# Performance work log

Hardware: AMD Instinct MI355X
Metric: run time of the kernel (lower is better)

## Reference

```python
import jax, jax.numpy as jnp
import numpy as np
from jax import lax

D_MODEL = 1024
D_STATE = 16
D_CONV = 4
EXPAND = 2
D_INNER = EXPAND * D_MODEL           # 2048 (mamba inner)
DT_RANK = (D_MODEL + 15) // 16       # 64
D_FF = 4 * D_MODEL                   # 4096 (SwiGLU hidden)
EPS = 1e-5
B, L = 2, 2048


def setup_inputs() -> dict:
    key = jax.random.key(0)
    ks = jax.random.split(key, 16)
    s = 0.02
    inp = {
        'x': jax.random.normal(ks[0], (B, L, D_MODEL), jnp.float32),
        'norm1_w': jnp.ones((D_MODEL,), jnp.float32),
        'norm2_w': jnp.ones((D_MODEL,), jnp.float32),
        # Mamba params (torch Linear convention: y = x @ W.T)
        'in_proj_w': s * jax.random.normal(ks[1], (2 * D_INNER, D_MODEL), jnp.float32),
        'conv_w': s * jax.random.normal(ks[2], (D_INNER, 1, D_CONV), jnp.float32),
        'conv_b': jnp.zeros((D_INNER,), jnp.float32),
        'x_proj_w': s * jax.random.normal(ks[3], (DT_RANK + 2 * D_STATE, D_INNER), jnp.float32),
        'dt_proj_w': s * jax.random.normal(ks[4], (D_INNER, DT_RANK), jnp.float32),
        'dt_proj_b': jax.random.uniform(ks[5], (D_INNER,), jnp.float32, -4.0, -2.0),
        'A_log': jnp.log(jnp.broadcast_to(jnp.arange(1, D_STATE + 1, dtype=jnp.float32), (D_INNER, D_STATE))),
        'D': jnp.ones((D_INNER,), jnp.float32),
        'out_proj_w': s * jax.random.normal(ks[6], (D_MODEL, D_INNER), jnp.float32),
        # SwiGLU MLP
        'w1': s * jax.random.normal(ks[7], (D_FF, D_MODEL), jnp.float32),
        'w2': s * jax.random.normal(ks[8], (D_FF, D_MODEL), jnp.float32),
        'w3': s * jax.random.normal(ks[9], (D_MODEL, D_FF), jnp.float32),
    }
    return inp


def _rmsnorm(x, w, eps=EPS):
    return x * lax.rsqrt(jnp.mean(x * x, axis=-1, keepdims=True) + eps) * w


def _mamba(x, in_proj_w, conv_w, conv_b, x_proj_w, dt_proj_w, dt_proj_b, A_log, Dp, out_proj_w):
    # x: (B, L, d_model)
    xz = x @ in_proj_w.T                       # (B, L, 2*d_inner)
    u, z = jnp.split(xz, 2, axis=-1)           # each (B, L, d_inner)
    # causal depthwise conv1d over time
    u_nch = u.transpose(0, 2, 1)               # (B, d_inner, L)
    u_conv = lax.conv_general_dilated(
        u_nch, conv_w, window_strides=(1,), padding=[(D_CONV - 1, 0)],
        dimension_numbers=('NCH', 'OIH', 'NCH'), feature_group_count=D_INNER)
    u_conv = u_conv + conv_b[None, :, None]
    u_act = jax.nn.silu(u_conv.transpose(0, 2, 1))   # (B, L, d_inner)
    # input-dependent dt, B, C
    proj = u_act @ x_proj_w.T                  # (B, L, dt_rank + 2*d_state)
    dt_r, Bm, Cm = jnp.split(proj, [DT_RANK, DT_RANK + D_STATE], axis=-1)
    dt = jax.nn.softplus(dt_r @ dt_proj_w.T + dt_proj_b)   # (B, L, d_inner)
    A = -jnp.exp(A_log)                        # (d_inner, d_state)
    dA = jnp.exp(jnp.einsum('bld,dn->bldn', dt, A))
    dBu = jnp.einsum('bld,bln,bld->bldn', dt, Bm, u_act)
    def step(h, inputs):
        dA_t, dBu_t = inputs                   # (B, d_inner, d_state)
        h = dA_t * h + dBu_t
        return h, h
    h0 = jnp.zeros((x.shape[0], D_INNER, D_STATE), x.dtype)
    _, hs = lax.scan(step, h0, (dA.transpose(1, 0, 2, 3), dBu.transpose(1, 0, 2, 3)))
    y = jnp.einsum('lbdn,bln->bld', hs, Cm) + u_act * Dp   # (B, L, d_inner)
    y = y * jax.nn.silu(z)
    return y @ out_proj_w.T                    # (B, L, d_model)


def reference(x, norm1_w, norm2_w, in_proj_w, conv_w, conv_b, x_proj_w,
              dt_proj_w, dt_proj_b, A_log, D, out_proj_w, w1, w2, w3):
    # residual + RMSNorm + Mamba (dropout = eval-mode identity)
    h = x + _mamba(_rmsnorm(x, norm1_w), in_proj_w, conv_w, conv_b,
                   x_proj_w, dt_proj_w, dt_proj_b, A_log, D, out_proj_w)
    # residual + RMSNorm + SwiGLU MLP
    xn = _rmsnorm(h, norm2_w)
    mlp = (jax.nn.silu(xn @ w1.T) * (xn @ w2.T)) @ w3.T
    return h + mlp
```

## Files before the change

### kernel.cpp

```cpp
#include <hip/hip_runtime.h>
#include <hip/hip_bf16.h>

#define TOKS 4096
#define DM   1024
#define DI   2048
#define DST  16
#define DTR  64
#define DFF  4096
#define PROJ_LD 128

#define NC    32
#define CHUNK 64

typedef __bf16 bf16x8 __attribute__((ext_vector_type(8)));
typedef float  f32x4  __attribute__((ext_vector_type(4)));

__device__ __forceinline__ __bf16 f2bf(float f) {
  union { float f; unsigned u; } v; v.f = f;
  unsigned r = v.u + 0x7fffu + ((v.u >> 16) & 1u);
  union { unsigned short s; __bf16 b; } o; o.s = (unsigned short)(r >> 16);
  return o.b;
}
__device__ __forceinline__ float siluf(float x) { return x / (1.f + __expf(-x)); }
__device__ __forceinline__ float softplusf(float x) { return x > 20.f ? x : log1pf(__expf(x)); }

__device__ __forceinline__ void gl2lds16(const void* g, void* l) {
  __builtin_amdgcn_global_load_lds((const __attribute__((address_space(1))) void*)g,
                                   (__attribute__((address_space(3))) void*)l, 16, 0, 0);
}

struct CvtArgs {
  const float* src[5];
  __bf16*      dst[5];
  int nblk[6];
};

__global__ __launch_bounds__(256) void cvt_bf16_kernel(CvtArgs a) {
  int blk = blockIdx.x;
  int seg = 0;
#pragma unroll
  for (int s = 1; s < 5; s++) if (blk >= a.nblk[s]) seg = s;
  size_t base = (size_t)(blk - a.nblk[seg]) * 2048 + threadIdx.x * 8;
  const float* src = a.src[seg] + base;
  __bf16*      dst = a.dst[seg] + base;
  float4 v0 = *(const float4*)src;
  float4 v1 = *(const float4*)(src + 4);
  union { __bf16 b[8]; uint4 u; } t;
  t.b[0]=f2bf(v0.x); t.b[1]=f2bf(v0.y); t.b[2]=f2bf(v0.z); t.b[3]=f2bf(v0.w);
  t.b[4]=f2bf(v1.x); t.b[5]=f2bf(v1.y); t.b[6]=f2bf(v1.z); t.b[7]=f2bf(v1.w);
  *(uint4*)dst = t.u;
}

__global__ __launch_bounds__(256) void cvt_w12_kernel(const float* __restrict__ w1,
                                                      const float* __restrict__ w2,
                                                      __bf16* __restrict__ dst) {
  int blk = blockIdx.x;
  int isw2 = blk >> 11;
  int b = blk & 2047;
  int r = b * 2 + (threadIdx.x >> 7);
  int col = (threadIdx.x & 127) * 8;
  const float* src = (isw2 ? w2 : w1) + (size_t)r * DM + col;
  int dr = (r >> 4) * 32 + (r & 15) + isw2 * 16;
  float4 v0 = *(const float4*)src;
  float4 v1 = *(const float4*)(src + 4);
  union { __bf16 b[8]; uint4 u; } t;
  t.b[0]=f2bf(v0.x); t.b[1]=f2bf(v0.y); t.b[2]=f2bf(v0.z); t.b[3]=f2bf(v0.w);
  t.b[4]=f2bf(v1.x); t.b[5]=f2bf(v1.y); t.b[6]=f2bf(v1.z); t.b[7]=f2bf(v1.w);
  *(uint4*)&dst[(size_t)dr * DM + col] = t.u;
}

__global__ __launch_bounds__(256) void rmsnorm_kernel(const float* __restrict__ x,
                                                      const float* __restrict__ w,
                                                      __bf16* __restrict__ out) {
  int row = blockIdx.x;
  const float* xr = x + (size_t)row * DM;
  float4 v = ((const float4*)xr)[threadIdx.x];
  float ss = v.x*v.x + v.y*v.y + v.z*v.z + v.w*v.w;
#pragma unroll
  for (int o = 32; o > 0; o >>= 1) ss += __shfl_xor(ss, o);
  __shared__ float sred[4];
  if ((threadIdx.x & 63) == 0) sred[threadIdx.x >> 6] = ss;
  __syncthreads();
  float tot = sred[0] + sred[1] + sred[2] + sred[3];
  float scale = rsqrtf(tot * (1.f / DM) + 1e-5f);
  float4 wv = ((const float4*)w)[threadIdx.x];
  union { __bf16 b[4]; ushort4 u; } o;
  o.b[0] = f2bf(v.x * scale * wv.x);
  o.b[1] = f2bf(v.y * scale * wv.y);
  o.b[2] = f2bf(v.z * scale * wv.z);
  o.b[3] = f2bf(v.w * scale * wv.w);
  *(ushort4*)&out[(size_t)row * DM + threadIdx.x * 4] = o.u;
}

template<int BM, int EPI, int SWAP, int KK, int Z, int LDA, int LDB, int LDC>
__global__ __launch_bounds__(256, BM == 256 ? 2 : 1) void gemm2(
    const void* __restrict__ Ap, const __bf16* __restrict__ Bp,
    void* __restrict__ Cp, const void* __restrict__ auxp)
{
  constexpr int FM = BM / 32;
  constexpr int AI = BM / 64;
  constexpr int kPer = KK / Z;
  __shared__ __bf16 sA[BM * 32];
  __shared__ __bf16 sB[128 * 32];
  const int tid  = threadIdx.x;
  const int wave = tid >> 6, lane = tid & 63;
  const int bm = SWAP ? blockIdx.x : blockIdx.y;
  const int bn = SWAP ? blockIdx.y : blockIdx.x;
  const int m0 = bm * BM, n0 = bn * 128;
  const int wr = wave >> 1, wc = wave & 1;
  const int frow = lane & 15, fq = lane >> 4;

  f32x4 acc[FM][4] = {};

  const int kBeg = (Z > 1) ? blockIdx.z * kPer : 0;
  const int kEnd = kBeg + kPer;

  const int lrow = lane >> 2;
  const int lcol = (lane & 3) * 8;

  for (int kt = kBeg; kt < kEnd; kt += 32) {
#pragma unroll
    for (int q = 0; q < AI; q++) {
      int idx = wave * AI + q;
      gl2lds16((const __bf16*)Ap + (size_t)(m0 + idx * 16 + lrow) * LDA + kt + lcol,
               &sA[idx * 512]);
    }
#pragma unroll
    for (int q = 0; q < 2; q++) {
      int idx = wave * 2 + q;
      gl2lds16(Bp + (size_t)(n0 + idx * 16 + lrow) * LDB + kt + lcol, &sB[idx * 512]);
    }
    __syncthreads();

    bf16x8 afr[FM], bfr[4];
#pragma unroll
    for (int i = 0; i < FM; i++)
      afr[i] = *(const bf16x8*)&sA[(wr * (BM/2) + i * 16 + frow) * 32 + fq * 8];
#pragma unroll
    for (int j = 0; j < 4; j++)
      bfr[j] = *(const bf16x8*)&sB[(wc * 64 + j * 16 + frow) * 32 + fq * 8];
#pragma unroll
    for (int i = 0; i < FM; i++)
#pragma unroll
      for (int j = 0; j < 4; j++)
        acc[i][j] = __builtin_amdgcn_mfma_f32_16x16x32_bf16(afr[i], bfr[j], acc[i][j], 0, 0, 0);
    __syncthreads();
  }

  const float* auxf = (const float*)auxp;
#pragma unroll
  for (int i = 0; i < FM; i++) {
    int gr = m0 + wr * (BM/2) + i * 16 + fq * 4;
#pragma unroll
    for (int j = 0; j < 4; j++) {
      int gc = n0 + wc * 64 + j * 16 + frow;
#pragma unroll
      for (int r = 0; r < 4; r++) {
        float v = acc[i][j][r];
        if (EPI == 6) {
          if (j & 1) {
            int col = (n0 >> 1) + 32 * wc + 16 * (j >> 1) + frow;
            size_t off = (size_t)(gr + r) * LDC + col;
            float g = acc[i][j-1][r];
            ((__bf16*)Cp)[off] = f2bf(siluf(g) * v);
          }
        } else {
          size_t off = (size_t)(gr + r) * LDC + gc;
          if (EPI == 1) ((__bf16*)Cp)[off] = f2bf(v);
          else if (EPI == 2) ((__bf16*)Cp)[off] = f2bf(softplusf(v + auxf[gc]));
          else if (EPI == 3) ((float*)Cp)[off] = v + auxf[off];
          else if (EPI == 7)
            ((float*)Cp)[(size_t)blockIdx.z * (TOKS * PROJ_LD) + off] = v;
        }
      }
    }
  }
}

__global__ __launch_bounds__(256) void xp_reduce_kernel(const float* __restrict__ part,
                                                        float* __restrict__ proj,
                                                        __bf16* __restrict__ projb) {
  int i = blockIdx.x * 256 + threadIdx.x;
  float4 s = ((const float4*)part)[i];
#pragma unroll
  for (int z = 1; z < 8; z++) {
    float4 v = ((const float4*)(part + (size_t)z * TOKS * PROJ_LD))[i];
    s.x += v.x; s.y += v.y; s.z += v.z; s.w += v.w;
  }
  ((float4*)proj)[i] = s;
  int c4 = i & 31;
  if (c4 < 16) {
    int tok = i >> 5;
    union { __bf16 b[4]; ushort4 u; } t;
    t.b[0]=f2bf(s.x); t.b[1]=f2bf(s.y); t.b[2]=f2bf(s.z); t.b[3]=f2bf(s.w);
    *(ushort4*)&projb[(size_t)tok * 64 + c4 * 4] = t.u;
  }
}

__global__ __launch_bounds__(256) void conv_silu_kernel(const __bf16* __restrict__ xz,
                                                        const float* __restrict__ cw,
                                                        const float* __restrict__ cb,
                                                        __bf16* __restrict__ uact) {
  int idx = blockIdx.x * 256 + threadIdx.x;
  int d   = idx & (DI - 1);
  int tok = idx >> 11;
  int l   = tok & 2047;
  float4 wv = *(const float4*)(cw + d * 4);
  const __bf16* up = xz + (size_t)tok * (2 * DI) + d;
  float acc = cb[d];
  if (l >= 3) acc += wv.x * (float)up[-3 * (2 * DI)];
  if (l >= 2) acc += wv.y * (float)up[-2 * (2 * DI)];
  if (l >= 1) acc += wv.z * (float)up[-1 * (2 * DI)];
  acc += wv.w * (float)up[0];
  uact[idx] = f2bf(siluf(acc));
}

__global__ __launch_bounds__(64) void scan_pass1(const __bf16* __restrict__ dt,
                                                 const __bf16* __restrict__ uact,
                                                 const float* __restrict__ proj,
                                                 const float* __restrict__ A_log,
                                                 float* __restrict__ aprod,
                                                 float* __restrict__ hend) {
  int lane = threadIdx.x;
  int d = blockIdx.x * 64 + lane;
  int c = blockIdx.y, b = blockIdx.z;
  float An[16], h[16], ap[16];
  {
    const float4* a4 = (const float4*)(A_log + (size_t)d * 16);
#pragma unroll
    for (int q = 0; q < 4; q++) {
      float4 v = a4[q];
      An[q*4+0] = -__expf(v.x); An[q*4+1] = -__expf(v.y);
      An[q*4+2] = -__expf(v.z); An[q*4+3] = -__expf(v.w);
    }
  }
#pragma unroll
  for (int n = 0; n < 16; n++) { h[n] = 0.f; ap[n] = 1.f; }

  size_t tok = (size_t)b * 2048 + (size_t)c * CHUNK;
  const __bf16* dtp = dt   + tok * DI + d;
  const __bf16* up  = uact + tok * DI + d;
  const float*  pp  = proj + tok * PROJ_LD;

  for (int t = 0; t < CHUNK; t++) {
    float dtv = (float)*dtp;
    float uv  = (float)*up;
    const float4* b4 = (const float4*)(pp + 64);
    float Bv[16];
#pragma unroll
    for (int q = 0; q < 4; q++) {
      float4 v = b4[q];
      Bv[q*4+0]=v.x; Bv[q*4+1]=v.y; Bv[q*4+2]=v.z; Bv[q*4+3]=v.w;
    }
    float du = dtv * uv;
#pragma unroll
    for (int n = 0; n < 16; n++) {
      float dA = __expf(dtv * An[n]);
      ap[n] *= dA;
      h[n] = fmaf(dA, h[n], du * Bv[n]);
    }
    dtp += DI; up += DI; pp += PROJ_LD;
  }

  size_t off = ((size_t)(b * NC + c) * DI + d) * 16;
#pragma unroll
  for (int q = 0; q < 4; q++) {
    *(float4*)(hend  + off + q*4) = make_float4(h[q*4+0],  h[q*4+1],  h[q*4+2],  h[q*4+3]);
    *(float4*)(aprod + off + q*4) = make_float4(ap[q*4+0], ap[q*4+1], ap[q*4+2], ap[q*4+3]);
  }
}

__global__ __launch_bounds__(256) void scan_pass2(const float* __restrict__ aprod,
                                                  const float* __restrict__ hend,
                                                  float* __restrict__ hstart) {
  int idx = blockIdx.x * 256 + threadIdx.x;
  int b  = idx >> 13;
  int r4 = idx & 8191;
  float4 H = make_float4(0.f, 0.f, 0.f, 0.f);
  for (int c = 0; c < NC; c++) {
    size_t off = (size_t)(b * NC + c) * (DI * 16 / 4) + r4;
    ((float4*)hstart)[off] = H;
    float4 a = ((const float4*)aprod)[off];
    float4 e = ((const float4*)hend)[off];
    H.x = fmaf(a.x, H.x, e.x);
    H.y = fmaf(a.y, H.y, e.y);
    H.z = fmaf(a.z, H.z, e.z);
    H.w = fmaf(a.w, H.w, e.w);
  }
}

__global__ __launch_bounds__(64) void scan_pass3(const __bf16* __restrict__ dt,
                                                 const __bf16* __restrict__ uact,
                                                 const float* __restrict__ proj,
                                                 const __bf16* __restrict__ xz,
                                                 const float* __restrict__ A_log,
                                                 const float* __restrict__ Dp,
                                                 const float* __restrict__ hstart,
                                                 __bf16* __restrict__ y) {
  int lane = threadIdx.x;
  int d = blockIdx.x * 64 + lane;
  int c = blockIdx.y, b = blockIdx.z;
  float An[16], h[16];
  {
    const float4* a4 = (const float4*)(A_log + (size_t)d * 16);
#pragma unroll
    for (int q = 0; q < 4; q++) {
      float4 v = a4[q];
      An[q*4+0] = -__expf(v.x); An[q*4+1] = -__expf(v.y);
      An[q*4+2] = -__expf(v.z); An[q*4+3] = -__expf(v.w);
    }
  }
  {
    size_t off = ((size_t)(b * NC + c) * DI + d) * 16;
#pragma unroll
    for (int q = 0; q < 4; q++) {
      float4 v = *(const float4*)(hstart + off + q*4);
      h[q*4+0]=v.x; h[q*4+1]=v.y; h[q*4+2]=v.z; h[q*4+3]=v.w;
    }
  }
  float Dd = Dp[d];

  size_t tok = (size_t)b * 2048 + (size_t)c * CHUNK;
  const __bf16* dtp = dt   + tok * DI + d;
  const __bf16* up  = uact + tok * DI + d;
  const float*  pp  = proj + tok * PROJ_LD;
  const __bf16* zp  = xz   + tok * (2 * DI) + DI + d;
  __bf16*       yp  = y    + tok * DI + d;

  for (int t = 0; t < CHUNK; t++) {
    float dtv = (float)*dtp;
    float uv  = (float)*up;
    float zv  = (float)*zp;
    const float4* b4 = (const float4*)(pp + 64);
    float Bv[16], Cv[16];
#pragma unroll
    for (int q = 0; q < 4; q++) {
      float4 v = b4[q];
      Bv[q*4+0]=v.x; Bv[q*4+1]=v.y; Bv[q*4+2]=v.z; Bv[q*4+3]=v.w;
      float4 w = b4[q + 4];
      Cv[q*4+0]=w.x; Cv[q*4+1]=w.y; Cv[q*4+2]=w.z; Cv[q*4+3]=w.w;
    }
    float du = dtv * uv;
    float p = 0.f;
#pragma unroll
    for (int n = 0; n < 16; n++) {
      float dA = __expf(dtv * An[n]);
      h[n] = fmaf(dA, h[n], du * Bv[n]);
      p = fmaf(h[n], Cv[n], p);
    }
    *yp = f2bf((p + Dd * uv) * siluf(zv));
    dtp += DI; up += DI; pp += PROJ_LD; zp += 2 * DI; yp += DI;
  }
}

extern "C" void kernel_launch(void* const* d_in, const int* in_sizes, int n_in,
                              void* d_out, int out_size, void* d_ws, size_t ws_size,
                              hipStream_t stream) {
  const float* x        = (const float*)d_in[0];
  const float* n1w      = (const float*)d_in[1];
  const float* n2w      = (const float*)d_in[2];
  const float* in_projw = (const float*)d_in[3];
  const float* conv_w   = (const float*)d_in[4];
  const float* conv_b   = (const float*)d_in[5];
  const float* x_projw  = (const float*)d_in[6];
  const float* dt_projw = (const float*)d_in[7];
  const float* dt_projb = (const float*)d_in[8];
  const float* A_log    = (const float*)d_in[9];
  const float* Dp       = (const float*)d_in[10];
  const float* out_projw= (const float*)d_in[11];
  const float* w1       = (const float*)d_in[12];
  const float* w2       = (const float*)d_in[13];
  const float* w3       = (const float*)d_in[14];
  float* out = (float*)d_out;

  char* ws = (char*)d_ws;
  __bf16* xz   = (__bf16*)(ws + 0);
  __bf16* uact = (__bf16*)(ws + 33554432);
  float*  proj = (float*) (ws + 50331648);
  __bf16* dt   = (__bf16*)(ws + 52428800);
  __bf16* yb   = (__bf16*)(ws + 85983232);
  float*  xpp  = (float*) (ws + 85983232);
  float*  h    = (float*) (ws + 102760448);
  __bf16* xn   = (__bf16*)(ws + 119537664);
  __bf16* hid  = xz;
  __bf16* projb = (__bf16*)(ws + 102760448);
  float* aprod  = (float*)(ws + 102760448);
  float* hend   = (float*)(ws + 111149056);
  float* hstart = (float*)(ws + 119537664);
  char* wb = ws + 127926272;
  __bf16* b_in  = (__bf16*)(wb);
  __bf16* b_xp  = (__bf16*)(wb + 8388608);
  __bf16* b_dtp = (__bf16*)(wb + 8912896);
  __bf16* b_out = (__bf16*)(wb + 9175040);
  __bf16* b_w12 = (__bf16*)(wb + 13369344);
  __bf16* b_w3  = (__bf16*)(wb + 30146560);

  hipMemsetAsync(b_xp, 0, 128 * 2048 * sizeof(__bf16), stream);

  CvtArgs ca;
  const float* srcs[5] = {in_projw, x_projw, dt_projw, out_projw, w3};
  __bf16* dsts[5]      = {b_in, b_xp, b_dtp, b_out, b_w3};
  int counts[5] = {4096*1024, 96*2048, 2048*64, 1024*2048, 1024*4096};
  int acc = 0;
  for (int i = 0; i < 5; i++) { ca.src[i] = srcs[i]; ca.dst[i] = dsts[i]; ca.nblk[i] = acc; acc += counts[i] / 2048; }
  ca.nblk[5] = acc;
  cvt_bf16_kernel<<<acc, 256, 0, stream>>>(ca);
  cvt_w12_kernel<<<4096, 256, 0, stream>>>(w1, w2, b_w12);

  dim3 blk(256);
  rmsnorm_kernel<<<TOKS, 256, 0, stream>>>(x, n1w, xn);
  gemm2<256,1,0, 1024,1, DM,DM,4096><<<dim3(32,16,1), blk, 0, stream>>>(xn, b_in, xz, nullptr);
  conv_silu_kernel<<<(TOKS*DI)/256, 256, 0, stream>>>(xz, conv_w, conv_b, uact);
  gemm2<128,7,0, 2048,8, DI,DI,PROJ_LD><<<dim3(1,32,8), blk, 0, stream>>>(uact, b_xp, xpp, nullptr);
  xp_reduce_kernel<<<512, 256, 0, stream>>>(xpp, proj, projb);
  gemm2<128,2,0, 64,1, 64,DTR,DI><<<dim3(16,32,1), blk, 0, stream>>>(projb, b_dtp, dt, dt_projb);
  scan_pass1<<<dim3(DI/64, NC, 2), 64, 0, stream>>>(dt, uact, proj, A_log, aprod, hend);
  scan_pass2<<<64, 256, 0, stream>>>(aprod, hend, hstart);
  scan_pass3<<<dim3(DI/64, NC, 2), 64, 0, stream>>>(dt, uact, proj, xz, A_log, Dp, hstart, yb);
  gemm2<128,3,1, 2048,1, DI,DI,DM><<<dim3(32,8,1), blk, 0, stream>>>(yb, b_out, h, x);
  rmsnorm_kernel<<<TOKS, 256, 0, stream>>>(h, n2w, xn);
  gemm2<256,6,0, 1024,1, DM,DM,DFF><<<dim3(64,16,1), blk, 0, stream>>>(xn, b_w12, hid, nullptr);
  gemm2<128,3,1, 4096,1, DFF,DFF,DM><<<dim3(32,8,1), blk, 0, stream>>>(hid, b_w3, out, h);

  (void)in_sizes; (void)n_in; (void)out_size; (void)ws_size;
}
```

Before: 562.7 us.

## Add 256x256 eight-wave ping-pong GEMM for in_proj and w1/w2 projections

Introduces a new GEMM kernel with 256x256 output tiles, 512 threads (8 waves), 128KB double-buffered LDS, swizzled layout, and an interleaved schedule of direct global-to-LDS loads, LDS fragment reads and MFMA blocks separated by barriers and s_setprio. It replaces the previous 256x128-ish gemm2 for the two large K=1024 projection GEMMs (in_proj and fused SwiGLU gate/up). The aim is higher arithmetic intensity per tile and better overlap of memory traffic with matrix-core work. It uses very large LDS per block, which limits occupancy, and fewer blocks, which may under-fill the CUs.

```diff
diff --git a/kernel.cpp b/kernel.cpp
--- a/kernel.cpp
+++ b/kernel.cpp
@@ -175,6 +175,165 @@
       }
     }
   }
+}
+
+template<int EPI, int KK, int LDA, int LDB, int LDC>
+__global__ __launch_bounds__(512, 2) void gemm8(
+    const __bf16* __restrict__ Ap, const __bf16* __restrict__ Bp,
+    void* __restrict__ Cp)
+{
+  constexpr int NT = KK / 64;
+  static_assert(NT % 2 == 0 && NT >= 2, "KK must be a multiple of 128");
+  __shared__ alignas(16) char S[131072];
+
+  const int tid  = threadIdx.x;
+  const int wid  = tid >> 6, lane = tid & 63;
+  const int wr   = wid >> 2, wc = wid & 3;
+  const int m0   = blockIdx.y * 256, n0 = blockIdx.x * 256;
+  const int frow = lane & 15, fq = lane >> 4;
+  const int cbyt = (fq * 16) ^ (((lane >> 3) & 1) << 5);
+  const int srow = lane >> 2;
+  const int skin = ((lane & 3) * 8) ^ (((lane >> 5) & 1) << 4);
+
+  f32x4 acc[2][2][4][2] = {};
+  bf16x8 fA[4][2], fB0[2][2], fB1[2][2];
+
+#define G8_STAGE(buf, ab, h, tile) do {                                        \
+    if ((tile) < NT) {                                                         \
+      const __bf16* gb = (ab) ? Bp : Ap;                                       \
+      const int ld = (ab) ? LDB : LDA;                                         \
+      const int r0 = ((ab) ? n0 : m0) + (h) * 128;                             \
+      _Pragma("unroll")                                                        \
+      for (int q = 0; q < 2; q++) {                                            \
+        int p = wid * 2 + q, kk = p >> 3, r16 = p & 7;                         \
+        const __bf16* src = gb + (size_t)(r0 + r16 * 16 + srow) * ld           \
+                            + (tile) * 64 + kk * 32 + skin;                    \
+        char* dst = S + (((buf) * 4 + (ab) * 2 + kk) << 14)                    \
+                    + ((h) * 128 + r16 * 16) * 64;                             \
+        gl2lds16(src, dst);                                                    \
+      }                                                                        \
+    }                                                                          \
+  } while (0)
+
+#define G8_READ_A(buf, mh) do {                                                \
+    _Pragma("unroll")                                                          \
+    for (int fi = 0; fi < 4; fi++)                                             \
+      _Pragma("unroll")                                                        \
+      for (int kk = 0; kk < 2; kk++)                                           \
+        fA[fi][kk] = *(const bf16x8*)(S + (((buf) * 4 + kk) << 14)             \
+            + ((mh) * 128 + wr * 64 + fi * 16 + frow) * 64 + cbyt);            \
+  } while (0)
+
+#define G8_READ_B(buf, nh, FB) do {                                            \
+    _Pragma("unroll")                                                          \
+    for (int fj = 0; fj < 2; fj++)                                             \
+      _Pragma("unroll")                                                        \
+      for (int kk = 0; kk < 2; kk++)                                           \
+        FB[fj][kk] = *(const bf16x8*)(S + (((buf) * 4 + 2 + kk) << 14)         \
+            + ((nh) * 128 + wc * 32 + fj * 16 + frow) * 64 + cbyt);            \
+  } while (0)
+
+#define G8_MFMA(mh, nh, FB) do {                                               \
+    __builtin_amdgcn_s_setprio(1);                                             \
+    _Pragma("unroll")                                                          \
+    for (int kk = 0; kk < 2; kk++)                                             \
+      _Pragma("unroll")                                                        \
+      for (int fi = 0; fi < 4; fi++)                                           \
+        _Pragma("unroll")                                                      \
+        for (int fj = 0; fj < 2; fj++)                                         \
+          acc[mh][nh][fi][fj] = __builtin_amdgcn_mfma_f32_16x16x32_bf16(       \
+              fA[fi][kk], FB[fj][kk], acc[mh][nh][fi][fj], 0, 0, 0);           \
+    __builtin_amdgcn_s_setprio(0);                                             \
+  } while (0)
+
+#define G8_BAR() do { asm volatile("" ::: "memory");                           \
+    __builtin_amdgcn_s_barrier(); asm volatile("" ::: "memory"); } while (0)
+#define G8_WAIT6() asm volatile("s_waitcnt vmcnt(6)" ::: "memory")
+#define G8_WAIT0() asm volatile("s_waitcnt vmcnt(0)" ::: "memory")
+
+  G8_STAGE(0, 0, 0, 0); G8_STAGE(0, 1, 1, 0); G8_STAGE(0, 0, 1, 0); G8_STAGE(0, 1, 0, 0);
+  G8_STAGE(1, 0, 0, 1); G8_STAGE(1, 1, 1, 1); G8_STAGE(1, 0, 1, 1);
+  G8_WAIT6();
+  G8_BAR();
+
+  for (int it = 0; it < NT / 2; ++it) {
+    const int t1 = 2 * it + 1, t2 = 2 * it + 2, t3 = 2 * it + 3;
+    const bool last = (it == NT / 2 - 1);
+    G8_READ_A(0, 0); G8_READ_B(0, 0, fB0);
+    G8_STAGE(1, 1, 0, t1);
+    G8_BAR();
+    G8_MFMA(0, 0, fB0);
+    G8_BAR();
+    G8_READ_B(0, 1, fB1);
+    G8_STAGE(0, 0, 0, t2);
+    G8_BAR();
+    G8_MFMA(0, 1, fB1);
+    G8_BAR();
+    G8_READ_A(0, 1);
+    G8_STAGE(0, 1, 1, t2);
+    G8_BAR();
+    G8_MFMA(1, 1, fB1);
+    G8_BAR();
+    G8_STAGE(0, 0, 1, t2);
+    if (last) G8_WAIT0(); else G8_WAIT6();
+    G8_BAR();
+    G8_MFMA(1, 0, fB0);
+    G8_BAR();
+    G8_READ_A(1, 0); G8_READ_B(1, 0, fB0);
+    G8_STAGE(0, 1, 0, t2);
+    G8_BAR();
+    G8_MFMA(0, 0, fB0);
+    G8_BAR();
+    G8_READ_B(1, 1, fB1);
+    G8_STAGE(1, 0, 0, t3);
+    G8_BAR();
+    G8_MFMA(0, 1, fB1);
+    G8_BAR();
+    G8_READ_A(1, 1);
+    G8_STAGE(1, 1, 1, t3);
+    G8_BAR();
+    G8_MFMA(1, 1, fB1);
+    G8_BAR();
+    G8_STAGE(1, 0, 1, t3);
+    if (!last) G8_WAIT6();
+    G8_BAR();
+    G8_MFMA(1, 0, fB0);
+    G8_BAR();
+  }
+
+#undef G8_STAGE
+#undef G8_READ_A
+#undef G8_READ_B
+#undef G8_MFMA
+#undef G8_BAR
+#undef G8_WAIT6
+#undef G8_WAIT0
+
+#pragma unroll
+  for (int mh = 0; mh < 2; mh++)
+#pragma unroll
+    for (int nh = 0; nh < 2; nh++)
+#pragma unroll
+      for (int fi = 0; fi < 4; fi++) {
+        int gr = m0 + mh * 128 + wr * 64 + fi * 16 + fq * 4;
+        if constexpr (EPI == 1) {
+#pragma unroll
+          for (int fj = 0; fj < 2; fj++) {
+            int gc = n0 + nh * 128 + wc * 32 + fj * 16 + frow;
+#pragma unroll
+            for (int r = 0; r < 4; r++)
+              ((__bf16*)Cp)[(size_t)(gr + r) * LDC + gc] = f2bf(acc[mh][nh][fi][fj][r]);
+          }
+        } else {
+          int col = ((n0 + nh * 128 + wc * 32) >> 1) + frow;
+#pragma unroll
+          for (int r = 0; r < 4; r++) {
+            float g = acc[mh][nh][fi][0][r];
+            float v = acc[mh][nh][fi][1][r];
+            ((__bf16*)Cp)[(size_t)(gr + r) * LDC + col] = f2bf(siluf(g) * v);
+          }
+        }
+      }
 }
 
 __global__ __launch_bounds__(256) void xp_reduce_kernel(const float* __restrict__ part,
@@ -409,7 +568,7 @@
 
   dim3 blk(256);
   rmsnorm_kernel<<<TOKS, 256, 0, stream>>>(x, n1w, xn);
-  gemm2<256,1,0, 1024,1, DM,DM,4096><<<dim3(32,16,1), blk, 0, stream>>>(xn, b_in, xz, nullptr);
+  gemm8<1, 1024, DM, DM, 4096><<<dim3(16, 16), 512, 0, stream>>>(xn, b_in, xz);
   conv_silu_kernel<<<(TOKS*DI)/256, 256, 0, stream>>>(xz, conv_w, conv_b, uact);
   gemm2<128,7,0, 2048,8, DI,DI,PROJ_LD><<<dim3(1,32,8), blk, 0, stream>>>(uact, b_xp, xpp, nullptr);
   xp_reduce_kernel<<<512, 256, 0, stream>>>(xpp, proj, projb);
@@ -419,7 +578,7 @@
   scan_pass3<<<dim3(DI/64, NC, 2), 64, 0, stream>>>(dt, uact, proj, xz, A_log, Dp, hstart, yb);
   gemm2<128,3,1, 2048,1, DI,DI,DM><<<dim3(32,8,1), blk, 0, stream>>>(yb, b_out, h, x);
   rmsnorm_kernel<<<TOKS, 256, 0, stream>>>(h, n2w, xn);
-  gemm2<256,6,0, 1024,1, DM,DM,DFF><<<dim3(64,16,1), blk, 0, stream>>>(xn, b_w12, hid, nullptr);
+  gemm8<6, 1024, DM, DM, DFF><<<dim3(32, 16), 512, 0, stream>>>(xn, b_w12, hid);
   gemm2<128,3,1, 4096,1, DFF,DFF,DM><<<dim3(32,8,1), blk, 0, stream>>>(hid, b_w3, out, h);
 
   (void)in_sizes; (void)n_in; (void)out_size; (void)ws_size;
```

After: 568.1 us. About the same (+1.0%).
